# Performance work log

Hardware: AMD Instinct MI355X
Metric: run time of the kernel (lower is better)

The kernel has to match this reference:

```python
import jax, jax.numpy as jnp
import numpy as np

N_HEADS = 8
NUM_CLASSES = 8
ATTN_INTENSE = 1.0


def setup_inputs() -> dict:
    key = jax.random.key(0)
    k1, k2, k3, k4 = jax.random.split(key, 4)
    bs, width, T = 8, 1536, 1024
    qkv = jax.random.normal(k1, (bs, width, T), dtype=jnp.float32)
    attn_mask = jax.random.randint(k2, (bs, 32, 32), 0, NUM_CLASSES, dtype=jnp.int32)
    # class embedding table: NUM_CLASSES rows + 1 null row (used for the global pass)
    embed_table = jax.random.normal(k3, (NUM_CLASSES + 1, 512), dtype=jnp.float32) * 0.02
    # Conv1d(embed_dim=512 -> 3*ch=192, kernel=1, bias=False) weight
    W_cls = jax.random.normal(k4, (192, 512), dtype=jnp.float32) * 0.02
    return {"qkv": qkv, "attn_mask": attn_mask, "embed_table": embed_table, "W_cls": W_cls}


def _attend(q, k, v, scale):
    # q,k,v: [B, T, C]; returns [B, T, C]
    logits = jnp.einsum('btc,bsc->bts', q * scale, k * scale)
    w = jax.nn.softmax(logits, axis=-1)
    return jnp.einsum('bts,bsc->btc', w, v)


def reference(qkv, attn_mask, embed_table, W_cls):
    bs, width, T = qkv.shape
    H = N_HEADS
    ch = width // (3 * H)            # 64
    scale = ch ** -0.25              # 1/sqrt(sqrt(ch))
    bH = bs * H

    qkv_h = qkv.reshape(bH, 3 * ch, T)
    q = jnp.transpose(qkv_h[:, 0 * ch:1 * ch], (0, 2, 1))  # [bH, T, ch]
    k = jnp.transpose(qkv_h[:, 1 * ch:2 * ch], (0, 2, 1))
    v = jnp.transpose(qkv_h[:, 2 * ch:3 * ch], (0, 2, 1))

    # ---- global pass with null class token ----
    null_tok = W_cls @ embed_table[NUM_CLASSES]  # [3*ch]
    qn, kn, vn = null_tok[:ch], null_tok[ch:2 * ch], null_tok[2 * ch:]
    a = _attend(q + qn, k + kn, v + vn, scale)   # [bH, T, ch]

    # ---- per-region (per segmentation class) attention ----
    seg = attn_mask.reshape(bs, T)
    segs = jnp.repeat(seg, H, axis=0)            # [bH, T], sample-major like qkv reshape

    out = a
    counter = jnp.ones((bH, T), dtype=qkv.dtype)
    for c in range(NUM_CLASSES):
        tok = W_cls @ embed_table[c]             # [3*ch], same token at every region position
        qc, kc, vc = tok[:ch], tok[ch:2 * ch], tok[2 * ch:]
        m = segs == c                            # [bH, T]
        logits = jnp.einsum('btc,bsc->bts', (q + qc) * scale, (k + kc) * scale)
        logits = jnp.where(m[:, None, :], logits, -1e9)   # restrict keys to region
        w = jax.nn.softmax(logits, axis=-1)
        a_c = jnp.einsum('bts,bsc->btc', w, v + vc)
        out = out + jnp.where(m[:, :, None], a_c, 0.0)    # scatter-add onto region queries
        counter = counter + ATTN_INTENSE * m.astype(counter.dtype)

    out = out / counter[:, :, None]              # [bH, T, ch]
    # faithful to original: outs are [ch, T] each, torch.stack(dim=1) -> [ch, bH, T], then reshape
    stacked = jnp.transpose(out, (2, 0, 1))      # [ch, bH, T]
    return stacked.reshape(bs, H * ch, T)
```

## Files before the change

### kernel.cpp

```cpp
#include <hip/hip_runtime.h>
#include <stdint.h>

typedef unsigned short u16;
typedef unsigned int   u32;
typedef __bf16 bf16_t;
typedef bf16_t bf16x8 __attribute__((ext_vector_type(8)));
typedef bf16_t bf16x2 __attribute__((ext_vector_type(2)));
typedef float  f32x2  __attribute__((ext_vector_type(2)));
typedef float  f32x4  __attribute__((ext_vector_type(4)));

#define QSCALE 0.18033688011112042f

__device__ __forceinline__ u32 pkbf(float a, float b) {
  f32x2 x = {a, b};
  bf16x2 y = __builtin_convertvector(x, bf16x2);
  union { bf16x2 v; u32 u; } c; c.v = y; return c.u;
}

__device__ __forceinline__ float fexp2(float x) {
#if __has_builtin(__builtin_amdgcn_exp2f)
  return __builtin_amdgcn_exp2f(x);
#else
  float r;
  asm("v_exp_f32 %0, %1\n\ts_nop 0" : "=v"(r) : "v"(x));
  return r;
#endif
}

__device__ __forceinline__ void gload_lds16(const void* g, void* l) {
  __builtin_amdgcn_global_load_lds(
      (const __attribute__((address_space(1))) void*)g,
      (__attribute__((address_space(3))) void*)l, 16, 0, 0);
}

__global__ void tok_kernel(const float* __restrict__ W, const float* __restrict__ E,
                           float* __restrict__ tok) {
  int c = blockIdx.x;
  int j = threadIdx.x;
  const f32x4* wr = (const f32x4*)(W + j * 512);
  const f32x4* er = (const f32x4*)(E + c * 512);
  float acc = 0.f;
  for (int i = 0; i < 128; ++i) {
    f32x4 w = wr[i], e = er[i];
    acc += w.x * e.x + w.y * e.y + w.z * e.z + w.w * e.w;
  }
  tok[c * 192 + j] = acc;
}

__global__ __launch_bounds__(256)
void prep_kernel(const float* __restrict__ qkv, const int* __restrict__ seg,
                 const float* __restrict__ tok, u16* __restrict__ tiles,
                 float* __restrict__ wtab) {
  __shared__ float part[256];
  const int B = blockIdx.x;
  const int tid = threadIdx.x;
  const int bh = B >> 4, kt = B & 15;
  const int s0 = kt * 64;
  const int b  = bh >> 3;
  const float* qg = qkv + (size_t)bh * 192 * 1024;
  u16* img = tiles + (size_t)B * 8192;
  {
    const int s = tid & 63, g = tid >> 6;
    const float* kb = qg + (size_t)(64 + g * 16) * 1024 + s0 + s;
    float kf[16];
#pragma unroll
    for (int i = 0; i < 16; ++i) kf[i] = kb[(size_t)i * 1024];
    u32 kp[8];
#pragma unroll
    for (int j2 = 0; j2 < 8; ++j2) kp[j2] = pkbf(kf[2 * j2], kf[2 * j2 + 1]);
    const int xr = (s & 7) << 3;
    *(uint4*)&img[s * 64 + ((g * 16)     ^ xr)] = make_uint4(kp[0], kp[1], kp[2], kp[3]);
    *(uint4*)&img[s * 64 + ((g * 16 + 8) ^ xr)] = make_uint4(kp[4], kp[5], kp[6], kp[7]);
    const int cs = seg[b * 1024 + s0 + s];
    const f32x4* tc = (const f32x4*)(tok + cs * 192 + g * 16);
    const f32x4* tn = (const f32x4*)(tok + 8 * 192 + g * 16);
    float pd = 0.f;
#pragma unroll
    for (int i = 0; i < 4; ++i) {
      f32x4 a = tc[i], n = tn[i];
      pd += (a.x - n.x) * kf[4 * i + 0] + (a.y - n.y) * kf[4 * i + 1] +
            (a.z - n.z) * kf[4 * i + 2] + (a.w - n.w) * kf[4 * i + 3];
    }
    part[s * 4 + g] = pd;
  }
  {
    const int g = tid & 15, dg = tid >> 4;
    const int cp = ((g >> 3) & 1) * 32 + (g & 3) * 8 + ((g >> 2) & 1) * 4;
    const float* vb = qg + (size_t)(128 + dg * 4) * 1024 + s0 + g * 4;
#pragma unroll
    for (int i = 0; i < 4; ++i) {
      f32x4 v = *(const f32x4*)(vb + (size_t)i * 1024);
      const int d = dg * 4 + i;
      *(uint2*)&img[4096 + d * 64 + (cp ^ ((d & 7) << 3))] =
          make_uint2(pkbf(v.x, v.y), pkbf(v.z, v.w));
    }
  }
  __syncthreads();
  if (tid < 64) {
    f32x4 p4 = *(const f32x4*)&part[tid * 4];
    wtab[(size_t)B * 64 + tid] = fexp2(QSCALE * ((p4.x + p4.y) + (p4.z + p4.w)));
  }
}

__global__ __launch_bounds__(256, 2)
void attn_kernel(const float* __restrict__ qkv, const int* __restrict__ seg,
                 const float* __restrict__ tok, const u16* __restrict__ tiles,
                 const float* __restrict__ wtab, float* __restrict__ out) {
  __shared__ __align__(16) u16 smem[16896];

  const int L  = blockIdx.x;
  const int bh = (L & 7) * 8 + ((L >> 3) & 7);
  const int qb = L >> 6;
  const int b  = bh >> 3;
  const int tid = threadIdx.x, wave = tid >> 6, lane = tid & 63;
  const int quad = lane >> 4, l16 = lane & 15;

  const float* qg   = qkv + (size_t)bh * 192 * 1024;
  const int*   segb = seg + b * 1024;
  const u16*   tbh  = tiles + (size_t)bh * (16 * 8192);
  const float* wbh  = wtab + (size_t)bh * (16 * 64);

  const int q0i = qb * 128 + wave * 32;
  const int tqA = q0i + l16, tqB = tqA + 16;
  const int mycA = segb[tqA], mycB = segb[tqB];
  int sqA[4], sqB[4];
#pragma unroll
  for (int r = 0; r < 4; ++r) {
    sqA[r] = segb[q0i + quad * 4 + r];
    sqB[r] = segb[q0i + 16 + quad * 4 + r];
  }

  const float* tn = tok + 8 * 192;
  union { u32 w[4]; bf16x8 v; } qA0[2], qB0[2];
#pragma unroll
  for (int kc = 0; kc < 2; ++kc)
#pragma unroll
    for (int jj = 0; jj < 4; ++jj) {
      int d = kc * 32 + quad * 8 + jj * 2;
      float a0 = qg[(size_t)d * 1024 + tqA];
      float a1 = qg[(size_t)(d + 1) * 1024 + tqA];
      float b0 = qg[(size_t)d * 1024 + tqB];
      float b1 = qg[(size_t)(d + 1) * 1024 + tqB];
      qA0[kc].w[jj] = pkbf((a0 + tn[d]) * QSCALE, (a1 + tn[d + 1]) * QSCALE);
      qB0[kc].w[jj] = pkbf((b0 + tn[d]) * QSCALE, (b1 + tn[d + 1]) * QSCALE);
    }

  f32x4 OA0[4], OAb[4], OB0[4], OBb[4];
#pragma unroll
  for (int dt = 0; dt < 4; ++dt) {
    OA0[dt] = (f32x4){0.f, 0.f, 0.f, 0.f};  OAb[dt] = (f32x4){0.f, 0.f, 0.f, 0.f};
    OB0[dt] = (f32x4){0.f, 0.f, 0.f, 0.f};  OBb[dt] = (f32x4){0.f, 0.f, 0.f, 0.f};
  }
  float rsA0 = 0.f, rsAb = 0.f, rsB0 = 0.f, rsBb = 0.f;

  {
    const char* src = (const char*)tbh + tid * 16;
    char* dst = (char*)smem + tid * 16;
#pragma unroll
    for (int i = 0; i < 4; ++i) gload_lds16(src + i * 4096, dst + i * 4096);
  }

  const int xq = (l16 & 7) << 3;

#pragma unroll 2
  for (int kt = 0; kt < 16; ++kt) {
    const int s0 = kt * 64;
    __syncthreads();
    if (kt + 1 < 16) {
      const char* src = (const char*)tbh + (size_t)(kt + 1) * 16384 + tid * 16;
      char* dst = (char*)smem + ((kt + 1) & 1) * 16384 + tid * 16;
#pragma unroll
      for (int i = 0; i < 4; ++i) gload_lds16(src + i * 4096, dst + i * 4096);
    }
    f32x4 wmA[4], wmB[4];
#pragma unroll
    for (int n4 = 0; n4 < 4; ++n4) {
      const int4  s4 = *(const int4*)&segb[s0 + n4 * 16 + quad * 4];
      const f32x4 wv = *(const f32x4*)&wbh[s0 + n4 * 16 + quad * 4];
      wmA[n4][0] = (s4.x == mycA) ? wv[0] : 0.f;
      wmA[n4][1] = (s4.y == mycA) ? wv[1] : 0.f;
      wmA[n4][2] = (s4.z == mycA) ? wv[2] : 0.f;
      wmA[n4][3] = (s4.w == mycA) ? wv[3] : 0.f;
      wmB[n4][0] = (s4.x == mycB) ? wv[0] : 0.f;
      wmB[n4][1] = (s4.y == mycB) ? wv[1] : 0.f;
      wmB[n4][2] = (s4.z == mycB) ? wv[2] : 0.f;
      wmB[n4][3] = (s4.w == mycB) ? wv[3] : 0.f;
    }

    const u16* ktr = smem + (kt & 1) * 8192;
    const u16* vls = ktr + 4096;

    f32x4 SA[4], SB[4];
#pragma unroll
    for (int n4 = 0; n4 < 4; ++n4) {
      const int srow = n4 * 16 + l16;
      f32x4 a0 = {0.f, 0.f, 0.f, 0.f}, c0 = {0.f, 0.f, 0.f, 0.f};
#pragma unroll
      for (int kc = 0; kc < 2; ++kc) {
        bf16x8 kfr = *(const bf16x8*)&ktr[srow * 64 + ((kc * 32 + quad * 8) ^ xq)];
        a0 = __builtin_amdgcn_mfma_f32_16x16x32_bf16(kfr, qA0[kc].v, a0, 0, 0, 0);
        c0 = __builtin_amdgcn_mfma_f32_16x16x32_bf16(kfr, qB0[kc].v, c0, 0, 0, 0);
      }
      SA[n4] = a0; SB[n4] = c0;
    }

    union { u32 w[4]; bf16x8 v; } paA0[2], paAb[2], paB0[2], paBb[2];
#define SOFTMAX_PACK(S, wm, rs0, rsb, pa0, pab)                                \
    {                                                                          \
      float p0[4][4], pb[4][4];                                                \
      _Pragma("unroll")                                                        \
      for (int n4 = 0; n4 < 4; ++n4)                                           \
        _Pragma("unroll")                                                      \
        for (int r = 0; r < 4; ++r) {                                          \
          p0[n4][r] = fexp2(S[n4][r]);                                         \
          pb[n4][r] = p0[n4][r] * wm[n4][r];                                   \
        }                                                                      \
      _Pragma("unroll")                                                        \
      for (int n4 = 0; n4 < 4; ++n4) {                                         \
        rs0 += (p0[n4][0] + p0[n4][1]) + (p0[n4][2] + p0[n4][3]);              \
        rsb += (pb[n4][0] + pb[n4][1]) + (pb[n4][2] + pb[n4][3]);              \
      }                                                                        \
      _Pragma("unroll")                                                        \
      for (int kc = 0; kc < 2; ++kc) {                                         \
        pa0[kc].w[0] = pkbf(p0[2 * kc][0],     p0[2 * kc][1]);                 \
        pa0[kc].w[1] = pkbf(p0[2 * kc][2],     p0[2 * kc][3]);                 \
        pa0[kc].w[2] = pkbf(p0[2 * kc + 1][0], p0[2 * kc + 1][1]);             \
        pa0[kc].w[3] = pkbf(p0[2 * kc + 1][2], p0[2 * kc + 1][3]);             \
        pab[kc].w[0] = pkbf(pb[2 * kc][0],     pb[2 * kc][1]);                 \
        pab[kc].w[1] = pkbf(pb[2 * kc][2],     pb[2 * kc][3]);                 \
        pab[kc].w[2] = pkbf(pb[2 * kc + 1][0], pb[2 * kc + 1][1]);             \
        pab[kc].w[3] = pkbf(pb[2 * kc + 1][2], pb[2 * kc + 1][3]);             \
      }                                                                        \
    }
    SOFTMAX_PACK(SA, wmA, rsA0, rsAb, paA0, paAb)
    SOFTMAX_PACK(SB, wmB, rsB0, rsBb, paB0, paBb)
#undef SOFTMAX_PACK

#pragma unroll
    for (int kc = 0; kc < 2; ++kc) {
      const int co = (kc * 32 + quad * 8) ^ xq;
#pragma unroll
      for (int dt = 0; dt < 4; ++dt) {
        bf16x8 vfr = *(const bf16x8*)&vls[(dt * 16 + l16) * 64 + co];
        OA0[dt] = __builtin_amdgcn_mfma_f32_16x16x32_bf16(paA0[kc].v, vfr, OA0[dt], 0, 0, 0);
        OAb[dt] = __builtin_amdgcn_mfma_f32_16x16x32_bf16(paAb[kc].v, vfr, OAb[dt], 0, 0, 0);
        OB0[dt] = __builtin_amdgcn_mfma_f32_16x16x32_bf16(paB0[kc].v, vfr, OB0[dt], 0, 0, 0);
        OBb[dt] = __builtin_amdgcn_mfma_f32_16x16x32_bf16(paBb[kc].v, vfr, OBb[dt], 0, 0, 0);
      }
    }
  }

  rsA0 += __shfl_xor(rsA0, 16, 64);  rsA0 += __shfl_xor(rsA0, 32, 64);
  rsAb += __shfl_xor(rsAb, 16, 64);  rsAb += __shfl_xor(rsAb, 32, 64);
  rsB0 += __shfl_xor(rsB0, 16, 64);  rsB0 += __shfl_xor(rsB0, 32, 64);
  rsBb += __shfl_xor(rsBb, 16, 64);  rsBb += __shfl_xor(rsBb, 32, 64);
  float invA0[4], invAb[4], invB0[4], invBb[4];
#pragma unroll
  for (int r = 0; r < 4; ++r) {
    float a0 = __shfl(rsA0, quad * 4 + r, 16);
    float ab = __shfl(rsAb, quad * 4 + r, 16);
    float b0 = __shfl(rsB0, quad * 4 + r, 16);
    float bb = __shfl(rsBb, quad * 4 + r, 16);
    invA0[r] = (a0 > 0.f) ? 1.f / a0 : 0.f;
    invAb[r] = (ab > 0.f) ? 1.f / ab : 0.f;
    invB0[r] = (b0 > 0.f) ? 1.f / b0 : 0.f;
    invBb[r] = (bb > 0.f) ? 1.f / bb : 0.f;
  }

  __syncthreads();
  float* fbuf = (float*)smem;
  const float* tvn = tok + 8 * 192 + 128;
#pragma unroll
  for (int dt = 0; dt < 4; ++dt) {
    const int d = dt * 16 + l16;
    const float bn = tvn[d];
    f32x4 wA, wB;
#pragma unroll
    for (int r = 0; r < 4; ++r) {
      float bcA = tok[sqA[r] * 192 + 128 + d];
      float bcB = tok[sqB[r] * 192 + 128 + d];
      wA[r] = 0.5f * (OA0[dt][r] * invA0[r] + bn + OAb[dt][r] * invAb[r] + bcA);
      wB[r] = 0.5f * (OB0[dt][r] * invB0[r] + bn + OBb[dt][r] * invBb[r] + bcB);
    }
    *(f32x4*)&fbuf[d * 132 + wave * 32 + quad * 4]      = wA;
    *(f32x4*)&fbuf[d * 132 + wave * 32 + 16 + quad * 4] = wB;
  }
  __syncthreads();
  {
    const size_t obase = (size_t)bh * 1024 + qb * 128;
    for (int i = tid; i < 8192; i += 256) {
      int d = i >> 7, t = i & 127;
      out[(size_t)d * 65536 + obase + t] = fbuf[d * 132 + t];
    }
  }
}

extern "C" void kernel_launch(void* const* d_in, const int* in_sizes, int n_in,
                              void* d_out, int out_size, void* d_ws, size_t ws_size,
                              hipStream_t stream) {
  (void)in_sizes; (void)n_in; (void)out_size; (void)ws_size;
  const float* qkv   = (const float*)d_in[0];
  const int*   amask = (const int*)d_in[1];
  const float* emb   = (const float*)d_in[2];
  const float* wcls  = (const float*)d_in[3];
  float* tok   = (float*)d_ws;
  u16*   tiles = (u16*)((char*)d_ws + 8192);
  float* wtab  = (float*)((char*)d_ws + 8192 + 16 * 1024 * 1024);
  float* out = (float*)d_out;

  hipLaunchKernelGGL(tok_kernel, dim3(9), dim3(192), 0, stream, wcls, emb, tok);
  hipLaunchKernelGGL(prep_kernel, dim3(1024), dim3(256), 0, stream,
                     qkv, amask, tok, tiles, wtab);
  hipLaunchKernelGGL(attn_kernel, dim3(512), dim3(256), 0, stream,
                     qkv, amask, tok, tiles, wtab, out);
}
```

Measured before the change: 145.3 us.

## Split key range across two wave groups in attention and parallelize token GEMV

The attention kernel now runs 512 threads per block. Two halves of four waves each process disjoint halves of the key tiles, using separate double-buffered LDS regions, and then combine row sums and partial outputs through shared memory. This is meant to shorten the serial key loop per block and raise wave-level parallelism, at the cost of doubled LDS use, extra barriers and the reduction. The tiny token kernel is also rewritten to use one wave per output with a shuffle reduction, replacing the serial 512-long loop per thread.

```diff
diff --git a/kernel.cpp b/kernel.cpp
--- a/kernel.cpp
+++ b/kernel.cpp
@@ -33,18 +33,23 @@
       (__attribute__((address_space(3))) void*)l, 16, 0, 0);
 }
 
-__global__ void tok_kernel(const float* __restrict__ W, const float* __restrict__ E,
-                           float* __restrict__ tok) {
-  int c = blockIdx.x;
-  int j = threadIdx.x;
-  const f32x4* wr = (const f32x4*)(W + j * 512);
-  const f32x4* er = (const f32x4*)(E + c * 512);
+__global__ __launch_bounds__(256)
+void tok_kernel(const float* __restrict__ W, const float* __restrict__ E,
+                float* __restrict__ tok) {
+  const int gw = blockIdx.x * 4 + (threadIdx.x >> 6);
+  const int lane = threadIdx.x & 63;
+  const int c = gw / 192, j = gw - c * 192;
+  const f32x4* w4 = (const f32x4*)(W + (size_t)j * 512) + lane * 2;
+  const f32x4* e4 = (const f32x4*)(E + (size_t)c * 512) + lane * 2;
   float acc = 0.f;
-  for (int i = 0; i < 128; ++i) {
-    f32x4 w = wr[i], e = er[i];
+#pragma unroll
+  for (int i = 0; i < 2; ++i) {
+    f32x4 w = w4[i], e = e4[i];
     acc += w.x * e.x + w.y * e.y + w.z * e.z + w.w * e.w;
   }
-  tok[c * 192 + j] = acc;
+#pragma unroll
+  for (int off = 32; off; off >>= 1) acc += __shfl_xor(acc, off, 64);
+  if (lane == 0) tok[c * 192 + j] = acc;
 }
 
 __global__ __launch_bounds__(256)
@@ -102,25 +107,28 @@
   }
 }
 
-__global__ __launch_bounds__(256, 2)
+__global__ __launch_bounds__(512, 4)
 void attn_kernel(const float* __restrict__ qkv, const int* __restrict__ seg,
                  const float* __restrict__ tok, const u16* __restrict__ tiles,
                  const float* __restrict__ wtab, float* __restrict__ out) {
-  __shared__ __align__(16) u16 smem[16896];
+  __shared__ __align__(16) u16 smem[32768];
 
   const int L  = blockIdx.x;
   const int bh = (L & 7) * 8 + ((L >> 3) & 7);
   const int qb = L >> 6;
   const int b  = bh >> 3;
-  const int tid = threadIdx.x, wave = tid >> 6, lane = tid & 63;
+  const int tid = threadIdx.x;
+  const int wave = tid >> 6, lane = tid & 63;
+  const int half = wave >> 2, qwave = wave & 3;
   const int quad = lane >> 4, l16 = lane & 15;
+  const int tid256 = tid & 255;
 
   const float* qg   = qkv + (size_t)bh * 192 * 1024;
   const int*   segb = seg + b * 1024;
   const u16*   tbh  = tiles + (size_t)bh * (16 * 8192);
   const float* wbh  = wtab + (size_t)bh * (16 * 64);
 
-  const int q0i = qb * 128 + wave * 32;
+  const int q0i = qb * 128 + qwave * 32;
   const int tqA = q0i + l16, tqB = tqA + 16;
   const int mycA = segb[tqA], mycB = segb[tqB];
   int sqA[4], sqB[4];
@@ -154,8 +162,8 @@
   float rsA0 = 0.f, rsAb = 0.f, rsB0 = 0.f, rsBb = 0.f;
 
   {
-    const char* src = (const char*)tbh + tid * 16;
-    char* dst = (char*)smem + tid * 16;
+    const char* src = (const char*)tbh + (size_t)(half * 8) * 16384 + tid256 * 16;
+    char* dst = (char*)smem + half * 32768 + tid256 * 16;
 #pragma unroll
     for (int i = 0; i < 4; ++i) gload_lds16(src + i * 4096, dst + i * 4096);
   }
@@ -163,12 +171,13 @@
   const int xq = (l16 & 7) << 3;
 
 #pragma unroll 2
-  for (int kt = 0; kt < 16; ++kt) {
+  for (int j = 0; j < 8; ++j) {
+    const int kt = half * 8 + j;
     const int s0 = kt * 64;
     __syncthreads();
-    if (kt + 1 < 16) {
-      const char* src = (const char*)tbh + (size_t)(kt + 1) * 16384 + tid * 16;
-      char* dst = (char*)smem + ((kt + 1) & 1) * 16384 + tid * 16;
+    if (j + 1 < 8) {
+      const char* src = (const char*)tbh + (size_t)(kt + 1) * 16384 + tid256 * 16;
+      char* dst = (char*)smem + half * 32768 + ((j + 1) & 1) * 16384 + tid256 * 16;
 #pragma unroll
       for (int i = 0; i < 4; ++i) gload_lds16(src + i * 4096, dst + i * 4096);
     }
@@ -187,7 +196,7 @@
       wmB[n4][3] = (s4.w == mycB) ? wv[3] : 0.f;
     }
 
-    const u16* ktr = smem + (kt & 1) * 8192;
+    const u16* ktr = smem + half * 16384 + (j & 1) * 8192;
     const u16* vls = ktr + 4096;
 
     f32x4 SA[4], SB[4];
@@ -254,41 +263,77 @@
   rsAb += __shfl_xor(rsAb, 16, 64);  rsAb += __shfl_xor(rsAb, 32, 64);
   rsB0 += __shfl_xor(rsB0, 16, 64);  rsB0 += __shfl_xor(rsB0, 32, 64);
   rsBb += __shfl_xor(rsBb, 16, 64);  rsBb += __shfl_xor(rsBb, 32, 64);
+
+  __syncthreads();
+  float* rsbuf = (float*)((char*)smem + 61440);
+  if (lane < 16) {
+    const int base = (half * 4 + qwave) * 64 + l16;
+    rsbuf[base +  0] = rsA0;
+    rsbuf[base + 16] = rsAb;
+    rsbuf[base + 32] = rsB0;
+    rsbuf[base + 48] = rsBb;
+  }
+  __syncthreads();
+  float tA0, tAb, tB0, tBb;
+  {
+    const int r0 = qwave * 64 + l16, r1 = (4 + qwave) * 64 + l16;
+    tA0 = rsbuf[r0 +  0] + rsbuf[r1 +  0];
+    tAb = rsbuf[r0 + 16] + rsbuf[r1 + 16];
+    tB0 = rsbuf[r0 + 32] + rsbuf[r1 + 32];
+    tBb = rsbuf[r0 + 48] + rsbuf[r1 + 48];
+  }
   float invA0[4], invAb[4], invB0[4], invBb[4];
 #pragma unroll
   for (int r = 0; r < 4; ++r) {
-    float a0 = __shfl(rsA0, quad * 4 + r, 16);
-    float ab = __shfl(rsAb, quad * 4 + r, 16);
-    float b0 = __shfl(rsB0, quad * 4 + r, 16);
-    float bb = __shfl(rsBb, quad * 4 + r, 16);
+    float a0 = __shfl(tA0, quad * 4 + r, 16);
+    float ab = __shfl(tAb, quad * 4 + r, 16);
+    float b0 = __shfl(tB0, quad * 4 + r, 16);
+    float bb = __shfl(tBb, quad * 4 + r, 16);
     invA0[r] = (a0 > 0.f) ? 1.f / a0 : 0.f;
     invAb[r] = (ab > 0.f) ? 1.f / ab : 0.f;
     invB0[r] = (b0 > 0.f) ? 1.f / b0 : 0.f;
     invBb[r] = (bb > 0.f) ? 1.f / bb : 0.f;
   }
 
-  __syncthreads();
   float* fbuf = (float*)smem;
   const float* tvn = tok + 8 * 192 + 128;
-#pragma unroll
-  for (int dt = 0; dt < 4; ++dt) {
-    const int d = dt * 16 + l16;
-    const float bn = tvn[d];
-    f32x4 wA, wB;
-#pragma unroll
-    for (int r = 0; r < 4; ++r) {
-      float bcA = tok[sqA[r] * 192 + 128 + d];
-      float bcB = tok[sqB[r] * 192 + 128 + d];
-      wA[r] = 0.5f * (OA0[dt][r] * invA0[r] + bn + OAb[dt][r] * invAb[r] + bcA);
-      wB[r] = 0.5f * (OB0[dt][r] * invB0[r] + bn + OBb[dt][r] * invBb[r] + bcB);
-    }
-    *(f32x4*)&fbuf[d * 132 + wave * 32 + quad * 4]      = wA;
-    *(f32x4*)&fbuf[d * 132 + wave * 32 + 16 + quad * 4] = wB;
+  if (half == 0) {
+#pragma unroll
+    for (int dt = 0; dt < 4; ++dt) {
+      const int d = dt * 16 + l16;
+      const float bn = tvn[d];
+      f32x4 wA, wB;
+#pragma unroll
+      for (int r = 0; r < 4; ++r) {
+        float bcA = tok[sqA[r] * 192 + 128 + d];
+        float bcB = tok[sqB[r] * 192 + 128 + d];
+        wA[r] = 0.5f * (OA0[dt][r] * invA0[r] + OAb[dt][r] * invAb[r] + bn + bcA);
+        wB[r] = 0.5f * (OB0[dt][r] * invB0[r] + OBb[dt][r] * invBb[r] + bn + bcB);
+      }
+      *(f32x4*)&fbuf[d * 132 + qwave * 32 + quad * 4]      = wA;
+      *(f32x4*)&fbuf[d * 132 + qwave * 32 + 16 + quad * 4] = wB;
+    }
+  }
+  __syncthreads();
+  if (half == 1) {
+#pragma unroll
+    for (int dt = 0; dt < 4; ++dt) {
+      const int d = dt * 16 + l16;
+      f32x4 wA = *(const f32x4*)&fbuf[d * 132 + qwave * 32 + quad * 4];
+      f32x4 wB = *(const f32x4*)&fbuf[d * 132 + qwave * 32 + 16 + quad * 4];
+#pragma unroll
+      for (int r = 0; r < 4; ++r) {
+        wA[r] += 0.5f * (OA0[dt][r] * invA0[r] + OAb[dt][r] * invAb[r]);
+        wB[r] += 0.5f * (OB0[dt][r] * invB0[r] + OBb[dt][r] * invBb[r]);
+      }
+      *(f32x4*)&fbuf[d * 132 + qwave * 32 + quad * 4]      = wA;
+      *(f32x4*)&fbuf[d * 132 + qwave * 32 + 16 + quad * 4] = wB;
+    }
   }
   __syncthreads();
   {
     const size_t obase = (size_t)bh * 1024 + qb * 128;
-    for (int i = tid; i < 8192; i += 256) {
+    for (int i = tid; i < 8192; i += 512) {
       int d = i >> 7, t = i & 127;
       out[(size_t)d * 65536 + obase + t] = fbuf[d * 132 + t];
     }
@@ -308,9 +353,9 @@
   float* wtab  = (float*)((char*)d_ws + 8192 + 16 * 1024 * 1024);
   float* out = (float*)d_out;
 
-  hipLaunchKernelGGL(tok_kernel, dim3(9), dim3(192), 0, stream, wcls, emb, tok);
+  hipLaunchKernelGGL(tok_kernel, dim3(432), dim3(256), 0, stream, wcls, emb, tok);
   hipLaunchKernelGGL(prep_kernel, dim3(1024), dim3(256), 0, stream,
                      qkv, amask, tok, tiles, wtab);
-  hipLaunchKernelGGL(attn_kernel, dim3(512), dim3(256), 0, stream,
+  hipLaunchKernelGGL(attn_kernel, dim3(512), dim3(512), 0, stream,
                      qkv, amask, tok, tiles, wtab, out);
 }
```

After: 297.4 us. 105% more time.
